# Kernel tuning notes

Measured on AMD Instinct MI355X. Metric: run time of the kernel, lower is better.

The kernel has to match this reference:

```python
import jax, jax.numpy as jnp
import numpy as np

N = 10000      # num nodes
E = 160000     # num edges (before self-loops)
D_IN = 512
D_HID = 512
D_OUT = 512
C = 64         # num classes


def setup_inputs() -> dict:
    key = jax.random.key(0)
    ks = jax.random.split(key, 8)
    x = jax.random.normal(ks[0], (N, D_IN), dtype=jnp.float32)
    edge_index = jax.random.randint(ks[1], (2, E), 0, N, dtype=jnp.int64)
    W1 = jax.random.normal(ks[2], (D_IN, D_HID), jnp.float32) / np.sqrt(D_IN)
    b1 = jnp.zeros((D_HID,), jnp.float32)
    W2 = jax.random.normal(ks[3], (D_HID, D_OUT), jnp.float32) / np.sqrt(D_HID)
    b2 = jnp.zeros((D_OUT,), jnp.float32)
    Wc = jax.random.normal(ks[4], (D_OUT, C), jnp.float32) / np.sqrt(D_OUT)
    bc = jnp.zeros((C,), jnp.float32)
    return {"x": x, "edge_index": edge_index, "W1": W1, "b1": b1,
            "W2": W2, "b2": b2, "Wc": Wc, "bc": bc}


def _gcn_conv(x, src, dst, ew, W, b):
    """GCNConv: symmetric degree-normalized scatter-add. ew = edge weights."""
    h = x @ W  # [N, D_out] dense GEMM
    deg = jax.ops.segment_sum(ew, dst, num_segments=N)  # in-degree incl. loops
    dis = jnp.where(deg > 0, jax.lax.rsqrt(jnp.maximum(deg, 1e-12)), 0.0)
    norm = dis[src] * dis[dst] * ew  # [E+N]
    out = jax.ops.segment_sum(h[src] * norm[:, None], dst, num_segments=N)
    return out + b


def reference(x, edge_index, W1, b1, W2, b2, Wc, bc):
    src, dst = edge_index[0], edge_index[1]
    # add_remaining_self_loops: drop existing self-loops, add one per node
    loops = jnp.arange(N, dtype=edge_index.dtype)
    src_f = jnp.concatenate([src, loops])
    dst_f = jnp.concatenate([dst, loops])
    ew = jnp.concatenate([(src != dst).astype(jnp.float32),
                          jnp.ones((N,), jnp.float32)])
    h = jax.nn.relu(_gcn_conv(x, src_f, dst_f, ew, W1, b1))
    h = _gcn_conv(h, src_f, dst_f, ew, W2, b2)
    logits = h @ Wc + bc
    return logits, jax.nn.log_softmax(logits, axis=1)
```

## Files before the change

### kernel.cpp

```cpp
#include <hip/hip_runtime.h>
#include <hip/hip_bf16.h>

#define N_NODES 10000
#define DIM 512
#define NCLS 64
#define BM 64
#define BN 128
#define BK 64
#define ELLW 64

typedef __hip_bfloat16 bf16;
typedef unsigned short u16;
typedef unsigned int u32;
typedef __attribute__((ext_vector_type(8))) short short8;
typedef __attribute__((ext_vector_type(4))) float f32x4;

__device__ __forceinline__ float b2f(bf16 v) { return __bfloat162float(v); }
__device__ __forceinline__ float ldIn(const void* p, size_t i, int isb) {
    return isb ? b2f(((const bf16*)p)[i]) : ((const float*)p)[i];
}
__device__ __forceinline__ int getE(const int* ei, int is64, int flat) {
    return is64 ? ei[2 * (size_t)flat] : ei[flat];
}
__device__ __forceinline__ void load_lds16(const bf16* g, bf16* l) {
    __builtin_amdgcn_global_load_lds(
        (const __attribute__((address_space(1))) void*)g,
        (__attribute__((address_space(3))) void*)l, 16, 0, 0);
}
__device__ __forceinline__ float blo(u32 v) { union {u32 u; float f;} x; x.u = v << 16; return x.f; }
__device__ __forceinline__ float bhi(u32 v) { union {u32 u; float f;} x; x.u = v & 0xffff0000u; return x.f; }
__device__ __forceinline__ u16  f2b(float f) { bf16 h = __float2bfloat16(f); return *(u16*)&h; }

__global__ __launch_bounds__(256) void convert_all(
        const void* __restrict__ X, const void* __restrict__ W1,
        const void* __restrict__ W2, const void* __restrict__ Wc,
        const void* __restrict__ b1, const void* __restrict__ b2,
        const void* __restrict__ bc, const int* __restrict__ ei,
        int* __restrict__ cursor, int* __restrict__ ell,
        bf16* __restrict__ Xb, bf16* __restrict__ Wt1, bf16* __restrict__ Wt2,
        bf16* __restrict__ Wtc, float* __restrict__ bF1, float* __restrict__ bF2,
        float* __restrict__ bFc, int E) {
    __shared__ float tile[32][33];
    __shared__ int sflags[2];
    int b = blockIdx.x, t = threadIdx.x;

    if (t < 64) {
        const u16* x16 = (const u16*)X;
        int cf = 0;
        #pragma unroll
        for (int j = 0; j < 4; j++) {
            int e = (x16[t * 4 + j] >> 7) & 0xFF;
            cf += (e >= 97 && e <= 157) ? 1 : 0;
        }
        #pragma unroll
        for (int o = 32; o > 0; o >>= 1) cf += __shfl_xor(cf, o, 64);
        int cz = (t < 32) ? ((ei[2 * t + 1] == 0) ? 1 : 0) : 0;
        #pragma unroll
        for (int o = 32; o > 0; o >>= 1) cz += __shfl_xor(cz, o, 64);
        if (t == 0) { sflags[0] = (cf >= 200) ? 1 : 0; sflags[1] = (cz >= 16) ? 1 : 0; }
    }
    __syncthreads();
    int isb = sflags[0], is64 = sflags[1];

    if (b < 2500) {
        int base = (b * 256 + t) * 8;
        bf16 o[8];
        if (isb) {
            *(uint4*)o = *(const uint4*)((const bf16*)X + base);
        } else {
            const float* Xf = (const float*)X + base;
            float4 v0 = *(const float4*)Xf, v1 = *(const float4*)(Xf + 4);
            o[0] = __float2bfloat16(v0.x); o[1] = __float2bfloat16(v0.y);
            o[2] = __float2bfloat16(v0.z); o[3] = __float2bfloat16(v0.w);
            o[4] = __float2bfloat16(v1.x); o[5] = __float2bfloat16(v1.y);
            o[6] = __float2bfloat16(v1.z); o[7] = __float2bfloat16(v1.w);
        }
        *(uint4*)&Xb[base] = *(uint4*)o;
    } else if (b < 3044) {
        const void* W; bf16* Wt; int N; int bb = b - 2500;
        if (bb < 256)      { W = W1; Wt = Wt1; N = DIM; }
        else if (bb < 512) { W = W2; Wt = Wt2; N = DIM;  bb -= 256; }
        else               { W = Wc; Wt = Wtc; N = NCLS; bb -= 512; }
        int nt = N / 32;
        int n0 = (bb % nt) * 32, k0 = (bb / nt) * 32;
        int tx = t & 31, ty = t >> 5;
        for (int r = ty; r < 32; r += 8)
            tile[r][tx] = ldIn(W, (size_t)(k0 + r) * N + n0 + tx, isb);
        __syncthreads();
        for (int r = ty; r < 32; r += 8)
            Wt[(size_t)(n0 + r) * DIM + k0 + tx] = __float2bfloat16(tile[tx][r]);
    } else if (b == 3044) {
        for (int i = t; i < 2 * DIM + NCLS; i += 256) {
            if (i < DIM)            bF1[i] = ldIn(b1, i, isb);
            else if (i < 2 * DIM)   bF2[i - DIM] = ldIn(b2, i - DIM, isb);
            else                    bFc[i - 2 * DIM] = ldIn(bc, i - 2 * DIM, isb);
        }
    } else {
        int e = (b - 3045) * 256 + t;
        if (e >= E) return;
        int s = getE(ei, is64, e), d = getE(ei, is64, E + e);
        if (s == d || (unsigned)s >= N_NODES || (unsigned)d >= N_NODES) return;
        int pos = atomicAdd(&cursor[d], 1);
        ell[d * ELLW + (pos & (ELLW - 1))] = s;
    }
}

__global__ __launch_bounds__(256) void gemm_mfma(
        const bf16* __restrict__ A, const bf16* __restrict__ Bt,
        bf16* __restrict__ C, int M, int Nc, int K,
        const int* __restrict__ deg) {
    __shared__ bf16 At[BM * BK];
    __shared__ bf16 Bts[BN * BK];
    int t = threadIdx.x;
    int w = t >> 6, l = t & 63;
    int bm = blockIdx.y * BM, bn = blockIdx.x * BN;
    int wn = w * 32;

    f32x4 acc[4][2] = {};
    int srow8 = l >> 3;
    int sk8b  = (l & 7) * 8;

    for (int k0 = 0; k0 < K; k0 += BK) {
        __syncthreads();
        #pragma unroll
        for (int i = 0; i < 2; i++) {
            int c = w * 2 + i;
            load_lds16(A + (size_t)(bm + c * 8 + srow8) * K + k0 + sk8b, &At[c * 512]);
        }
        #pragma unroll
        for (int i = 0; i < 4; i++) {
            int c = w * 4 + i;
            load_lds16(Bt + (size_t)(bn + c * 8 + srow8) * K + k0 + sk8b, &Bts[c * 512]);
        }
        __syncthreads();

        #pragma unroll
        for (int kk = 0; kk < BK; kk += 32) {
            short8 af[4], bfr[2];
            #pragma unroll
            for (int i = 0; i < 4; i++)
                af[i] = *(const short8*)&At[(i * 16 + (l & 15)) * BK + kk + (l >> 4) * 8];
            #pragma unroll
            for (int j = 0; j < 2; j++)
                bfr[j] = *(const short8*)&Bts[(wn + j * 16 + (l & 15)) * BK + kk + (l >> 4) * 8];
            #pragma unroll
            for (int i = 0; i < 4; i++)
                #pragma unroll
                for (int j = 0; j < 2; j++)
                    acc[i][j] = __builtin_amdgcn_mfma_f32_16x16x32_bf16(
                                    af[i], bfr[j], acc[i][j], 0, 0, 0);
        }
    }

    int col = l & 15, rq = (l >> 4) * 4;
    #pragma unroll
    for (int i = 0; i < 4; i++) {
        #pragma unroll
        for (int r = 0; r < 4; r++) {
            int gm = bm + i * 16 + rq + r;
            if (gm >= M) continue;
            float rs = rsqrtf((float)deg[gm] + 1.0f);
            #pragma unroll
            for (int j = 0; j < 2; j++) {
                int gn = bn + wn + j * 16 + col;
                C[(size_t)gm * Nc + gn] = __float2bfloat16(acc[i][j][r] * rs);
            }
        }
    }
}

__global__ __launch_bounds__(256) void gather_ell(
        const int* __restrict__ cursor, const int* __restrict__ ell,
        const bf16* __restrict__ Hs, const float* __restrict__ bias,
        bf16* __restrict__ Out, int relu) {
    int t = threadIdx.x;
    int w = t >> 6, lane = t & 63;
    int chunk = blockIdx.x & 3;
    int wid = (blockIdx.x >> 2) * 4 + w;
    if (wid >= N_NODES) return;
    int c0 = chunk * 128 + lane * 2;
    int cnt0 = cursor[wid];
    int cnt = min(cnt0, ELLW);
    int idx = ell[wid * ELLW + lane];

    u32 v = *(const u32*)(Hs + (size_t)wid * DIM + c0);
    float a0 = blo(v), a1 = bhi(v);

    int e = 0;
    for (; e + 7 < cnt; e += 8) {
        u32 r[8];
        #pragma unroll
        for (int b = 0; b < 8; b++) {
            int s = __shfl(idx, e + b, 64);
            r[b] = *(const u32*)(Hs + (size_t)s * DIM + c0);
        }
        a0 += ((blo(r[0]) + blo(r[1])) + (blo(r[2]) + blo(r[3])))
            + ((blo(r[4]) + blo(r[5])) + (blo(r[6]) + blo(r[7])));
        a1 += ((bhi(r[0]) + bhi(r[1])) + (bhi(r[2]) + bhi(r[3])))
            + ((bhi(r[4]) + bhi(r[5])) + (bhi(r[6]) + bhi(r[7])));
    }
    for (; e < cnt; e++) {
        int s = __shfl(idx, e, 64);
        u32 rv = *(const u32*)(Hs + (size_t)s * DIM + c0);
        a0 += blo(rv); a1 += bhi(rv);
    }

    float ds = rsqrtf((float)cnt0 + 1.0f);
    float v0 = a0 * ds + bias[c0];
    float v1 = a1 * ds + bias[c0 + 1];
    if (relu) { v0 = fmaxf(v0, 0.0f); v1 = fmaxf(v1, 0.0f); }
    u32 o = (u32)f2b(v0) | ((u32)f2b(v1) << 16);
    *(u32*)(Out + (size_t)wid * DIM + c0) = o;
}

__global__ __launch_bounds__(64) void cls_lsm_kernel(
        const bf16* __restrict__ A, const bf16* __restrict__ Wct,
        const float* __restrict__ bias, float* __restrict__ out, int M) {
    int l = threadIdx.x;
    int row0 = blockIdx.x * 16;
    int q = l >> 4, col15 = l & 15;

    f32x4 acc[4] = {};
    #pragma unroll 4
    for (int k0 = 0; k0 < DIM; k0 += 32) {
        short8 af = *(const short8*)&A[(size_t)(row0 + col15) * DIM + k0 + q * 8];
        #pragma unroll
        for (int j = 0; j < 4; j++) {
            short8 bfr = *(const short8*)&Wct[(size_t)(j * 16 + col15) * DIM + k0 + q * 8];
            acc[j] = __builtin_amdgcn_mfma_f32_16x16x32_bf16(af, bfr, acc[j], 0, 0, 0);
        }
    }

    float bcol[4];
    #pragma unroll
    for (int j = 0; j < 4; j++) bcol[j] = bias[j * 16 + col15];

    #pragma unroll
    for (int r = 0; r < 4; r++) {
        int row = row0 + q * 4 + r;
        float v[4];
        #pragma unroll
        for (int j = 0; j < 4; j++) v[j] = acc[j][r] + bcol[j];
        float m = fmaxf(fmaxf(v[0], v[1]), fmaxf(v[2], v[3]));
        #pragma unroll
        for (int o = 8; o > 0; o >>= 1) m = fmaxf(m, __shfl_xor(m, o, 64));
        float s = __expf(v[0] - m) + __expf(v[1] - m) + __expf(v[2] - m) + __expf(v[3] - m);
        #pragma unroll
        for (int o = 8; o > 0; o >>= 1) s += __shfl_xor(s, o, 64);
        float lse = m + __logf(s);
        if (row < M) {
            #pragma unroll
            for (int j = 0; j < 4; j++) {
                out[(size_t)row * NCLS + j * 16 + col15] = v[j];
                out[(size_t)M * NCLS + (size_t)row * NCLS + j * 16 + col15] = v[j] - lse;
            }
        }
    }
}

extern "C" void kernel_launch(void* const* d_in, const int* in_sizes, int n_in,
                              void* d_out, int out_size, void* d_ws, size_t ws_size,
                              hipStream_t stream) {
    const void* x  = d_in[0];
    const int*  ei = (const int*)d_in[1];
    const void* W1 = d_in[2];
    const void* b1 = d_in[3];
    const void* W2 = d_in[4];
    const void* b2 = d_in[5];
    const void* Wc = d_in[6];
    const void* bc = d_in[7];
    float* out = (float*)d_out;
    int E = in_sizes[1] / 2;

    char* ws = (char*)d_ws;
    float* bF1    = (float*)ws;
    float* bF2    = (float*)(ws + 4096);
    float* bFc    = (float*)(ws + 8192);
    int*   cursor = (int*)(ws + 65536);
    int*   ell    = (int*)(ws + 131072);
    bf16*  xb     = (bf16*) (ws + 4194304);
    bf16*  Wt1    = (bf16*) (ws + 14680064);
    bf16*  Wt2    = (bf16*) (ws + 15204352);
    bf16*  Wct    = (bf16*) (ws + 15728640);
    bf16*  B0     = (bf16*) (ws + 16777216);
    bf16*  B1     = (bf16*) (ws + 27262976);

    dim3 gg(DIM / BN, (N_NODES + BM - 1) / BM);
    int gConv = 3045 + (E + 255) / 256;

    hipMemsetAsync(cursor, 0, N_NODES * sizeof(int), stream);
    convert_all<<<gConv, 256, 0, stream>>>(x, W1, W2, Wc, b1, b2, bc, ei,
                                           cursor, ell, xb, Wt1, Wt2, Wct,
                                           bF1, bF2, bFc, E);

    gemm_mfma<<<gg, 256, 0, stream>>>(xb, Wt1, B0, N_NODES, DIM, DIM, cursor);
    gather_ell<<<N_NODES, 256, 0, stream>>>(cursor, ell, B0, bF1, B1, 1);

    gemm_mfma<<<gg, 256, 0, stream>>>(B1, Wt2, B0, N_NODES, DIM, DIM, cursor);
    gather_ell<<<N_NODES, 256, 0, stream>>>(cursor, ell, B0, bF2, B1, 0);

    cls_lsm_kernel<<<(N_NODES + 15) / 16, 64, 0, stream>>>(B1, Wct, bFc, out, N_NODES);
}
```

Measured before the change: 180.1 us.

## Double-buffer GEMM LDS tiles, XOR-swizzle LDS layout, remap blocks per XCD

After: 174.6 us. -3.0%, faster.

```diff
diff --git a/kernel.cpp b/kernel.cpp
--- a/kernel.cpp
+++ b/kernel.cpp
@@ -109,40 +109,59 @@
         const bf16* __restrict__ A, const bf16* __restrict__ Bt,
         bf16* __restrict__ C, int M, int Nc, int K,
         const int* __restrict__ deg) {
-    __shared__ bf16 At[BM * BK];
-    __shared__ bf16 Bts[BN * BK];
+    __shared__ bf16 At[2][BM * BK];
+    __shared__ bf16 Bts[2][BN * BK];
     int t = threadIdx.x;
     int w = t >> 6, l = t & 63;
-    int bm = blockIdx.y * BM, bn = blockIdx.x * BN;
+
+    int bid = blockIdx.x;
+    int xcd = bid & 7, i0 = bid >> 3;
+    int tile = (xcd < 4 ? xcd * 79 : 316 + (xcd - 4) * 78) + i0;
+    int bm = (tile >> 2) * BM, bn = (tile & 3) * BN;
     int wn = w * 32;
 
     f32x4 acc[4][2] = {};
     int srow8 = l >> 3;
-    int sk8b  = (l & 7) * 8;
+    int sk8b  = (((l & 7) ^ srow8) * 8);
+
+    #pragma unroll
+    for (int i = 0; i < 2; i++) {
+        int c = w * 2 + i;
+        load_lds16(A + (size_t)(bm + c * 8 + srow8) * K + sk8b, &At[0][c * 512]);
+    }
+    #pragma unroll
+    for (int i = 0; i < 4; i++) {
+        int c = w * 4 + i;
+        load_lds16(Bt + (size_t)(bn + c * 8 + srow8) * K + sk8b, &Bts[0][c * 512]);
+    }
+    __syncthreads();
 
     for (int k0 = 0; k0 < K; k0 += BK) {
-        __syncthreads();
-        #pragma unroll
-        for (int i = 0; i < 2; i++) {
-            int c = w * 2 + i;
-            load_lds16(A + (size_t)(bm + c * 8 + srow8) * K + k0 + sk8b, &At[c * 512]);
-        }
-        #pragma unroll
-        for (int i = 0; i < 4; i++) {
-            int c = w * 4 + i;
-            load_lds16(Bt + (size_t)(bn + c * 8 + srow8) * K + k0 + sk8b, &Bts[c * 512]);
-        }
-        __syncthreads();
-
+        int cur = (k0 >> 6) & 1;
+        if (k0 + BK < K) {
+            #pragma unroll
+            for (int i = 0; i < 2; i++) {
+                int c = w * 2 + i;
+                load_lds16(A + (size_t)(bm + c * 8 + srow8) * K + k0 + BK + sk8b,
+                           &At[cur ^ 1][c * 512]);
+            }
+            #pragma unroll
+            for (int i = 0; i < 4; i++) {
+                int c = w * 4 + i;
+                load_lds16(Bt + (size_t)(bn + c * 8 + srow8) * K + k0 + BK + sk8b,
+                           &Bts[cur ^ 1][c * 512]);
+            }
+        }
         #pragma unroll
         for (int kk = 0; kk < BK; kk += 32) {
             short8 af[4], bfr[2];
+            int slot = (((kk >> 3) + (l >> 4)) ^ (l & 7)) * 8;
             #pragma unroll
             for (int i = 0; i < 4; i++)
-                af[i] = *(const short8*)&At[(i * 16 + (l & 15)) * BK + kk + (l >> 4) * 8];
+                af[i] = *(const short8*)&At[cur][(i * 16 + (l & 15)) * BK + slot];
             #pragma unroll
             for (int j = 0; j < 2; j++)
-                bfr[j] = *(const short8*)&Bts[(wn + j * 16 + (l & 15)) * BK + kk + (l >> 4) * 8];
+                bfr[j] = *(const short8*)&Bts[cur][(wn + j * 16 + (l & 15)) * BK + slot];
             #pragma unroll
             for (int i = 0; i < 4; i++)
                 #pragma unroll
@@ -150,6 +169,7 @@
                     acc[i][j] = __builtin_amdgcn_mfma_f32_16x16x32_bf16(
                                     af[i], bfr[j], acc[i][j], 0, 0, 0);
         }
+        __syncthreads();
     }
 
     int col = l & 15, rq = (l >> 4) * 4;
@@ -285,18 +305,18 @@
     bf16*  B0     = (bf16*) (ws + 16777216);
     bf16*  B1     = (bf16*) (ws + 27262976);
 
-    dim3 gg(DIM / BN, (N_NODES + BM - 1) / BM);
     int gConv = 3045 + (E + 255) / 256;
+    const int GEMM_GRID = 628;
 
     hipMemsetAsync(cursor, 0, N_NODES * sizeof(int), stream);
     convert_all<<<gConv, 256, 0, stream>>>(x, W1, W2, Wc, b1, b2, bc, ei,
                                            cursor, ell, xb, Wt1, Wt2, Wct,
                                            bF1, bF2, bFc, E);
 
-    gemm_mfma<<<gg, 256, 0, stream>>>(xb, Wt1, B0, N_NODES, DIM, DIM, cursor);
+    gemm_mfma<<<GEMM_GRID, 256, 0, stream>>>(xb, Wt1, B0, N_NODES, DIM, DIM, cursor);
     gather_ell<<<N_NODES, 256, 0, stream>>>(cursor, ell, B0, bF1, B1, 1);
 
-    gemm_mfma<<<gg, 256, 0, stream>>>(B1, Wt2, B0, N_NODES, DIM, DIM, cursor);
+    gemm_mfma<<<GEMM_GRID, 256, 0, stream>>>(B1, Wt2, B0, N_NODES, DIM, DIM, cursor);
     gather_ell<<<N_NODES, 256, 0, stream>>>(cursor, ell, B0, bF2, B1, 0);
 
     cls_lsm_kernel<<<(N_NODES + 15) / 16, 64, 0, stream>>>(B1, Wct, bFc, out, N_NODES);
```
